# Kernel tuning notes

Measured on AMD Instinct MI355X. Metric: run time of the kernel, lower is better.

## Reference

```python
import jax, jax.numpy as jnp
import numpy as np

S = 2048  # expert group size
M = 768   # hidden size
H = 3072  # intermediate size
E = 16    # num experts


def top2_gating(gates):
    # gates: [G, S, E]
    G, S_, E_ = gates.shape
    C = 2 * S_ // E_
    mask_dtype = jnp.int32
    index_1 = jnp.argmax(gates, axis=-1)
    mask_1 = jax.nn.one_hot(index_1, E_, dtype=mask_dtype)
    gate_1 = jnp.einsum('GSE,GSE->GS', gates, mask_1)
    gates_without_top_1 = gates * (1 - mask_1)
    index_2 = jnp.argmax(gates_without_top_1, axis=-1)
    mask_2 = jax.nn.one_hot(index_2, E_, dtype=mask_dtype)
    gate_2 = jnp.einsum('GSE,GSE->GS', gates_without_top_1, mask_2)
    pos_1 = jnp.cumsum(mask_1, axis=-2) - mask_1
    mask_1 = mask_1 * (pos_1 < C)
    pos_1 = jnp.einsum('GSE,GSE->GS', pos_1, mask_1)
    mask_1_count = jnp.sum(mask_1, axis=-2)
    mask_1_flat = jnp.sum(mask_1, axis=-1)
    pos_2 = jnp.cumsum(mask_2, axis=-2) - mask_2 + jnp.expand_dims(mask_1_count, -2)
    mask_2 = mask_2 * (pos_2 < C)
    pos_2 = jnp.einsum('GSE,GSE->GS', pos_2, mask_2)
    mask_2_flat = jnp.sum(mask_2, axis=-1)
    gate_1 = gate_1 * mask_1_flat
    gate_2 = gate_2 * mask_2_flat
    denom = gate_1 + gate_2
    denom = jnp.where(denom > 0, denom, jnp.ones_like(denom))
    gate_1 = gate_1 / denom
    gate_2 = gate_2 / denom
    a = jnp.expand_dims(gate_1 * mask_1_flat, -1) * jax.nn.one_hot(index_1, E_, dtype=gates.dtype)
    b = jax.nn.one_hot(pos_1, C, dtype=gates.dtype)
    first = jnp.einsum('GSE,GSC->GSEC', a, b)
    a = jnp.expand_dims(gate_2 * mask_2_flat, -1) * jax.nn.one_hot(index_2, E_, dtype=gates.dtype)
    b = jax.nn.one_hot(pos_2, C, dtype=gates.dtype)
    second = jnp.einsum('GSE,GSC->GSEC', a, b)
    combined_tensor = first + second
    dispatch_tensor = combined_tensor.astype(jnp.bool_)
    return combined_tensor, dispatch_tensor


def setup_inputs() -> dict:
    key = jax.random.key(0)
    k1, k2, k3, k4 = jax.random.split(key, 4)
    inputs = jax.random.normal(k1, (4, 1024, M), dtype=jnp.float32)
    wg = jax.random.normal(k2, (M, E), dtype=jnp.float32) * (1.0 / np.sqrt(M))
    wi = jax.random.normal(k3, (E, M, H), dtype=jnp.float32) * (1.0 / np.sqrt(M))
    wo = jax.random.normal(k4, (E, H, M), dtype=jnp.float32) * (1.0 / np.sqrt(H))
    return {"inputs": inputs, "wg": wg, "wi": wi, "wo": wo}


def reference(inputs, wg, wi, wo):
    x = jnp.reshape(inputs, (-1, S, M))                      # [G, S, M]
    gates = jax.nn.softmax(jnp.einsum('GSM,ME->GSE', x, wg))
    combined_weights, dispatch_mask = top2_gating(gates)
    dispatched = jnp.einsum('GSEC,GSM->EGCM',
                            dispatch_mask.astype(x.dtype), x)
    h = jnp.einsum('EGCM,EMH->EGCH', dispatched, wi)
    h = jax.nn.relu(h)
    expert_out = jnp.einsum('EGCH,EHM->GECM', h, wo)
    out = jnp.einsum('GSEC,GECM->GSM', combined_weights, expert_out)
    return jnp.reshape(out, inputs.shape)
```

## Files before the change

kernel.cpp:

```cpp
#include <hip/hip_runtime.h>
#include <hip/hip_bf16.h>
#include <cstdint>
#include <cstddef>

#define S_TOK 2048
#define M_DIM 768
#define H_DIM 3072
#define E_NUM 16
#define CAP   256

using s16x8 = __attribute__((ext_vector_type(8))) short;
using f32x4 = __attribute__((ext_vector_type(4))) float;

__device__ __forceinline__ unsigned short f2bf(float f) {
    unsigned u = __float_as_uint(f);
    unsigned r = 0x7fffu + ((u >> 16) & 1u);
    return (unsigned short)((u + r) >> 16);
}

__device__ __forceinline__ void async16(const void* g, void* l) {
    __builtin_amdgcn_global_load_lds((const __attribute__((address_space(1))) void*)g,
                                     (__attribute__((address_space(3))) void*)l, 16, 0, 0);
}

__global__ void gating_kernel(const float* __restrict__ x, const float* __restrict__ wg,
                              int* __restrict__ e1o, int* __restrict__ e2o,
                              float* __restrict__ g1o, float* __restrict__ g2o, int ntok) {
    int gid  = blockIdx.x * blockDim.x + threadIdx.x;
    int tok  = gid >> 6;
    int lane = threadIdx.x & 63;
    if (tok >= ntok) return;
    const float* xr = x + (size_t)tok * M_DIM;
    float acc[E_NUM];
#pragma unroll
    for (int e = 0; e < E_NUM; ++e) acc[e] = 0.f;
    for (int m = lane; m < M_DIM; m += 64) {
        float xv = xr[m];
        const float* wr = wg + (size_t)m * E_NUM;
#pragma unroll
        for (int e = 0; e < E_NUM; ++e) acc[e] += xv * wr[e];
    }
#pragma unroll
    for (int off = 32; off >= 1; off >>= 1) {
#pragma unroll
        for (int e = 0; e < E_NUM; ++e) acc[e] += __shfl_xor(acc[e], off, 64);
    }
    if (lane == 0) {
        float mx = acc[0];
#pragma unroll
        for (int e = 1; e < E_NUM; ++e) mx = fmaxf(mx, acc[e]);
        float p[E_NUM]; float s = 0.f;
#pragma unroll
        for (int e = 0; e < E_NUM; ++e) { p[e] = expf(acc[e] - mx); s += p[e]; }
        float inv = 1.f / s;
        int b1 = 0; float v1 = -1.f;
#pragma unroll
        for (int e = 0; e < E_NUM; ++e) { if (p[e] > v1) { v1 = p[e]; b1 = e; } }
        int b2 = 0; float v2 = -1.f;
#pragma unroll
        for (int e = 0; e < E_NUM; ++e) { if (e != b1 && p[e] > v2) { v2 = p[e]; b2 = e; } }
        e1o[tok] = b1; e2o[tok] = b2;
        g1o[tok] = v1 * inv; g2o[tok] = v2 * inv;
    }
}

__global__ void assign_kernel(const int* __restrict__ e1a, const int* __restrict__ e2a,
                              const float* __restrict__ g1a, const float* __restrict__ g2a,
                              int* __restrict__ slot1, int* __restrict__ slot2,
                              float* __restrict__ w1, float* __restrict__ w2,
                              int* __restrict__ tfs, int G) {
    int g    = blockIdx.x;
    int tid  = threadIdx.x;
    int w    = tid >> 6;
    int lane = tid & 63;
    __shared__ int cnt1s[E_NUM];

    for (int i = tid; i < E_NUM * CAP; i += 1024) tfs[(size_t)g * E_NUM * CAP + i] = -1;
    __syncthreads();

    {
        int cnt = 0;
        for (int base = 0; base < S_TOK; base += 64) {
            int t = g * S_TOK + base + lane;
            bool pred = (e1a[t] == w);
            unsigned long long bal = __ballot(pred);
            int prefix = __popcll(bal & ((1ull << lane) - 1ull));
            if (pred) {
                int pos = cnt + prefix;
                if (pos < CAP) {
                    slot1[t] = w * CAP + pos;
                    tfs[((size_t)g * E_NUM + w) * CAP + pos] = base + lane;
                } else {
                    slot1[t] = -1;
                }
            }
            cnt += __popcll(bal);
        }
        if (lane == 0) cnt1s[w] = cnt < CAP ? cnt : CAP;
    }
    __syncthreads();
    {
        int cnt = cnt1s[w];
        for (int base = 0; base < S_TOK; base += 64) {
            int t = g * S_TOK + base + lane;
            bool pred = (e2a[t] == w);
            unsigned long long bal = __ballot(pred);
            int prefix = __popcll(bal & ((1ull << lane) - 1ull));
            if (pred) {
                int pos = cnt + prefix;
                if (pos < CAP) {
                    slot2[t] = w * CAP + pos;
                    tfs[((size_t)g * E_NUM + w) * CAP + pos] = base + lane;
                } else {
                    slot2[t] = -1;
                }
            }
            cnt += __popcll(bal);
        }
    }
    __syncthreads();
    for (int t = tid; t < S_TOK; t += 1024) {
        int gt = g * S_TOK + t;
        float a = slot1[gt] >= 0 ? g1a[gt] : 0.f;
        float b = slot2[gt] >= 0 ? g2a[gt] : 0.f;
        float denom = a + b;
        if (!(denom > 0.f)) denom = 1.f;
        w1[gt] = a / denom;
        w2[gt] = b / denom;
    }
}

__global__ void convert_x_kernel(const float* __restrict__ x, unsigned short* __restrict__ xb,
                                 int ntok) {
    int i4 = blockIdx.x * blockDim.x + threadIdx.x;
    size_t base = (size_t)i4 * 4;
    size_t n_real = (size_t)ntok * M_DIM;
    size_t n_tot  = (size_t)(ntok + 1) * M_DIM;
    if (base >= n_tot) return;
    ushort4 o;
    if (base < n_real) {
        float4 v = *(const float4*)&x[base];
        o.x = f2bf(v.x); o.y = f2bf(v.y); o.z = f2bf(v.z); o.w = f2bf(v.w);
    } else {
        o.x = o.y = o.z = o.w = 0;
    }
    *(ushort4*)&xb[base] = o;
}

__global__ __launch_bounds__(256) void transpose_conv_kernel(const float* __restrict__ src,
                                                             unsigned short* __restrict__ dst,
                                                             int R, int C) {
    __shared__ float T[64][65];
    int e  = blockIdx.z;
    int c0 = blockIdx.x * 64;
    int r0 = blockIdx.y * 64;
    int tid = threadIdx.x;
    int lx = tid & 63, ly = tid >> 6;
    const float* S = src + (size_t)e * R * C;
#pragma unroll
    for (int i = 0; i < 16; ++i) {
        int r = i * 4 + ly;
        T[r][lx] = S[(size_t)(r0 + r) * C + c0 + lx];
    }
    __syncthreads();
    unsigned short* D = dst + (size_t)e * C * R;
#pragma unroll
    for (int i = 0; i < 16; ++i) {
        int c = i * 4 + ly;
        D[(size_t)(c0 + c) * R + r0 + lx] = f2bf(T[lx][c]);
    }
}

template<int KLEN, bool GATHER>
__global__ __launch_bounds__(256) void mfma_gemm_kernel(
        const unsigned short* __restrict__ A,
        const unsigned short* __restrict__ B,
        const int* __restrict__ tfs,
        void* __restrict__ Out, int G, int N_total) {
    __shared__ unsigned short As[128 * 32];
    __shared__ unsigned short Bs[128 * 32];
    __shared__ int rowtok[128];

    int z  = blockIdx.z;
    int e  = z / G, g = z % G;
    int n0 = blockIdx.x * 128;
    int c0 = blockIdx.y * 128;
    int tid = threadIdx.x;

    if (GATHER) {
        if (tid < 128) rowtok[tid] = tfs[((size_t)g * E_NUM + e) * CAP + c0 + tid];
        __syncthreads();
    }

    int r4 = tid >> 2, l4 = tid & 3;
    const unsigned short *apt0, *apt1;
    if (GATHER) {
        int t0 = rowtok[r4], t1 = rowtok[64 + r4];
        size_t row0 = (t0 < 0) ? (size_t)(G * S_TOK) : (size_t)(g * S_TOK + t0);
        size_t row1 = (t1 < 0) ? (size_t)(G * S_TOK) : (size_t)(g * S_TOK + t1);
        apt0 = A + row0 * KLEN + l4 * 8;
        apt1 = A + row1 * KLEN + l4 * 8;
    } else {
        apt0 = A + ((size_t)z * CAP + c0 + r4) * KLEN + l4 * 8;
        apt1 = apt0 + (size_t)64 * KLEN;
    }
    const unsigned short* Bexp = B + (size_t)e * N_total * KLEN;
    const unsigned short* bpt0 = Bexp + ((size_t)n0 + r4) * KLEN + l4 * 8;
    const unsigned short* bpt1 = bpt0 + (size_t)64 * KLEN;

    int wv = tid >> 6;
    unsigned short* as0 = &As[(wv * 16) * 32];
    unsigned short* as1 = &As[(64 + wv * 16) * 32];
    unsigned short* bs0 = &Bs[(wv * 16) * 32];
    unsigned short* bs1 = &Bs[(64 + wv * 16) * 32];

    int lane = tid & 63;
    int r = lane & 15, q = lane >> 4;
    int wm = wv & 1, wn = wv >> 1;

    f32x4 acc[4][4];
#pragma unroll
    for (int i = 0; i < 4; ++i)
#pragma unroll
        for (int j = 0; j < 4; ++j) acc[i][j] = (f32x4)(0.f);

    for (int k0 = 0; k0 < KLEN; k0 += 32) {
        async16(apt0, as0);
        async16(apt1, as1);
        async16(bpt0, bs0);
        async16(bpt1, bs1);
        apt0 += 32; apt1 += 32; bpt0 += 32; bpt1 += 32;
        __syncthreads();
        s16x8 af[4], bfr[4];
#pragma unroll
        for (int i = 0; i < 4; ++i)
            af[i] = *(const s16x8*)&As[(wm * 64 + i * 16 + r) * 32 + q * 8];
#pragma unroll
        for (int j = 0; j < 4; ++j)
            bfr[j] = *(const s16x8*)&Bs[(wn * 64 + j * 16 + r) * 32 + q * 8];
#pragma unroll
        for (int i = 0; i < 4; ++i)
#pragma unroll
            for (int j = 0; j < 4; ++j)
                acc[i][j] = __builtin_amdgcn_mfma_f32_16x16x32_bf16(af[i], bfr[j], acc[i][j], 0, 0, 0);
        __syncthreads();
    }

    if (GATHER) {
        unsigned short* H = (unsigned short*)Out;
#pragma unroll
        for (int i = 0; i < 4; ++i) {
#pragma unroll
            for (int v = 0; v < 4; ++v) {
                int m_loc = wm * 64 + i * 16 + q * 4 + v;
                unsigned short* row = H + ((size_t)z * CAP + c0 + m_loc) * N_total + n0;
#pragma unroll
                for (int j = 0; j < 4; ++j) {
                    int n_loc = wn * 64 + j * 16 + r;
                    row[n_loc] = f2bf(fmaxf(acc[i][j][v], 0.f));
                }
            }
        }
    } else {
        float* O = (float*)Out;
#pragma unroll
        for (int i = 0; i < 4; ++i) {
#pragma unroll
            for (int v = 0; v < 4; ++v) {
                int m_loc = wm * 64 + i * 16 + q * 4 + v;
                float* row = O + (((size_t)g * E_NUM + e) * CAP + c0 + m_loc) * N_total + n0;
#pragma unroll
                for (int j = 0; j < 4; ++j) {
                    int n_loc = wn * 64 + j * 16 + r;
                    row[n_loc] = acc[i][j][v];
                }
            }
        }
    }
}

__global__ void combine_kernel(const float* __restrict__ eo,
                               const int* __restrict__ slot1, const int* __restrict__ slot2,
                               const float* __restrict__ w1, const float* __restrict__ w2,
                               float* __restrict__ out, int G) {
    int t = blockIdx.x;
    int g = t / S_TOK;
    int tid = threadIdx.x;
    int s1 = slot1[t], s2 = slot2[t];
    float a = w1[t], b = w2[t];
    const float* base_g = eo + (size_t)g * E_NUM * CAP * M_DIM;
    const float* p1 = base_g + (size_t)(s1 < 0 ? 0 : s1) * M_DIM;
    const float* p2 = base_g + (size_t)(s2 < 0 ? 0 : s2) * M_DIM;
    for (int m = tid; m < M_DIM; m += 256) {
        float v = 0.f;
        if (s1 >= 0) v += a * p1[m];
        if (s2 >= 0) v += b * p2[m];
        out[(size_t)t * M_DIM + m] = v;
    }
}

extern "C" void kernel_launch(void* const* d_in, const int* in_sizes, int n_in,
                              void* d_out, int out_size, void* d_ws, size_t ws_size,
                              hipStream_t stream) {
    const float* x  = (const float*)d_in[0];
    const float* wg = (const float*)d_in[1];
    const float* wi = (const float*)d_in[2];
    const float* wo = (const float*)d_in[3];
    float* out = (float*)d_out;

    int ntok = in_sizes[0] / M_DIM;
    int G = ntok / S_TOK;

    char* wsp = (char*)d_ws;
    auto carve = [&](size_t bytes) {
        void* p = (void*)wsp;
        wsp += (bytes + 255) & ~(size_t)255;
        return p;
    };
    int*   e1    = (int*)carve((size_t)ntok * 4);
    int*   e2    = (int*)carve((size_t)ntok * 4);
    float* g1    = (float*)carve((size_t)ntok * 4);
    float* g2    = (float*)carve((size_t)ntok * 4);
    int*   slot1 = (int*)carve((size_t)ntok * 4);
    int*   slot2 = (int*)carve((size_t)ntok * 4);
    float* w1    = (float*)carve((size_t)ntok * 4);
    float* w2    = (float*)carve((size_t)ntok * 4);
    int*   tfs   = (int*)carve((size_t)G * E_NUM * CAP * 4);
    unsigned short* xb  = (unsigned short*)carve((size_t)(ntok + 1) * M_DIM * 2);
    unsigned short* wiT = (unsigned short*)carve((size_t)E_NUM * H_DIM * M_DIM * 2);
    unsigned short* woT = (unsigned short*)carve((size_t)E_NUM * M_DIM * H_DIM * 2);
    unsigned short* h   = (unsigned short*)carve((size_t)E_NUM * G * CAP * H_DIM * 2);
    float* eo = (float*)carve((size_t)G * E_NUM * CAP * M_DIM * 4);

    gating_kernel<<<(ntok * 64 + 255) / 256, 256, 0, stream>>>(x, wg, e1, e2, g1, g2, ntok);
    assign_kernel<<<G, 1024, 0, stream>>>(e1, e2, g1, g2, slot1, slot2, w1, w2, tfs, G);

    int nx4 = ((ntok + 1) * M_DIM) / 4;
    convert_x_kernel<<<(nx4 + 255) / 256, 256, 0, stream>>>(x, xb, ntok);
    transpose_conv_kernel<<<dim3(H_DIM / 64, M_DIM / 64, E_NUM), 256, 0, stream>>>(wi, wiT, M_DIM, H_DIM);
    transpose_conv_kernel<<<dim3(M_DIM / 64, H_DIM / 64, E_NUM), 256, 0, stream>>>(wo, woT, H_DIM, M_DIM);

    mfma_gemm_kernel<M_DIM, true><<<dim3(H_DIM / 128, CAP / 128, E_NUM * G), 256, 0, stream>>>(
        xb, wiT, tfs, h, G, H_DIM);
    mfma_gemm_kernel<H_DIM, false><<<dim3(M_DIM / 128, CAP / 128, E_NUM * G), 256, 0, stream>>>(
        h, woT, tfs, eo, G, M_DIM);

    combine_kernel<<<ntok, 256, 0, stream>>>(eo, slot1, slot2, w1, w2, out, G);
}
```

Measured before the change: 552.4 us.

## Fuse combine into second GEMM via atomics, split-K, fuse x conversion into gating

The second expert GEMM now splits K in two and atomically accumulates gate-weighted results directly into the output, removing the expert-output buffer and the combine kernel. A small zero kernel clears the output first. The bf16 conversion of x is folded into the gating kernel, and the first GEMM uses 256-row tiles with 512 threads to reuse weight tiles across capacity rows. This trades a buffer round trip and a few launches for float atomics, which are nondeterministic in summation order, and it hardcodes two groups in the grid indexing.

```diff
diff --git a/kernel.cpp b/kernel.cpp
--- a/kernel.cpp
+++ b/kernel.cpp
@@ -25,17 +25,24 @@
 
 __global__ void gating_kernel(const float* __restrict__ x, const float* __restrict__ wg,
                               int* __restrict__ e1o, int* __restrict__ e2o,
-                              float* __restrict__ g1o, float* __restrict__ g2o, int ntok) {
+                              float* __restrict__ g1o, float* __restrict__ g2o,
+                              unsigned short* __restrict__ xb, int ntok) {
+    if (blockIdx.x == 0) {
+        for (int m = threadIdx.x; m < M_DIM; m += blockDim.x)
+            xb[(size_t)ntok * M_DIM + m] = 0;
+    }
     int gid  = blockIdx.x * blockDim.x + threadIdx.x;
     int tok  = gid >> 6;
     int lane = threadIdx.x & 63;
     if (tok >= ntok) return;
     const float* xr = x + (size_t)tok * M_DIM;
+    unsigned short* xbr = xb + (size_t)tok * M_DIM;
     float acc[E_NUM];
 #pragma unroll
     for (int e = 0; e < E_NUM; ++e) acc[e] = 0.f;
     for (int m = lane; m < M_DIM; m += 64) {
         float xv = xr[m];
+        xbr[m] = f2bf(xv);
         const float* wr = wg + (size_t)m * E_NUM;
 #pragma unroll
         for (int e = 0; e < E_NUM; ++e) acc[e] += xv * wr[e];
@@ -67,7 +74,7 @@
 __global__ void assign_kernel(const int* __restrict__ e1a, const int* __restrict__ e2a,
                               const float* __restrict__ g1a, const float* __restrict__ g2a,
                               int* __restrict__ slot1, int* __restrict__ slot2,
-                              float* __restrict__ w1, float* __restrict__ w2,
+                              float* __restrict__ wslot,
                               int* __restrict__ tfs, int G) {
     int g    = blockIdx.x;
     int tid  = threadIdx.x;
@@ -79,10 +86,15 @@
     __syncthreads();
 
     {
+        int vals[S_TOK / 64];
+#pragma unroll
+        for (int it = 0; it < S_TOK / 64; ++it) vals[it] = e1a[g * S_TOK + it * 64 + lane];
         int cnt = 0;
-        for (int base = 0; base < S_TOK; base += 64) {
+#pragma unroll
+        for (int it = 0; it < S_TOK / 64; ++it) {
+            int base = it * 64;
             int t = g * S_TOK + base + lane;
-            bool pred = (e1a[t] == w);
+            bool pred = (vals[it] == w);
             unsigned long long bal = __ballot(pred);
             int prefix = __popcll(bal & ((1ull << lane) - 1ull));
             if (pred) {
@@ -100,10 +112,15 @@
     }
     __syncthreads();
     {
+        int vals[S_TOK / 64];
+#pragma unroll
+        for (int it = 0; it < S_TOK / 64; ++it) vals[it] = e2a[g * S_TOK + it * 64 + lane];
         int cnt = cnt1s[w];
-        for (int base = 0; base < S_TOK; base += 64) {
+#pragma unroll
+        for (int it = 0; it < S_TOK / 64; ++it) {
+            int base = it * 64;
             int t = g * S_TOK + base + lane;
-            bool pred = (e2a[t] == w);
+            bool pred = (vals[it] == w);
             unsigned long long bal = __ballot(pred);
             int prefix = __popcll(bal & ((1ull << lane) - 1ull));
             if (pred) {
@@ -121,30 +138,14 @@
     __syncthreads();
     for (int t = tid; t < S_TOK; t += 1024) {
         int gt = g * S_TOK + t;
-        float a = slot1[gt] >= 0 ? g1a[gt] : 0.f;
-        float b = slot2[gt] >= 0 ? g2a[gt] : 0.f;
+        int s1 = slot1[gt], s2 = slot2[gt];
+        float a = s1 >= 0 ? g1a[gt] : 0.f;
+        float b = s2 >= 0 ? g2a[gt] : 0.f;
         float denom = a + b;
         if (!(denom > 0.f)) denom = 1.f;
-        w1[gt] = a / denom;
-        w2[gt] = b / denom;
-    }
-}
-
-__global__ void convert_x_kernel(const float* __restrict__ x, unsigned short* __restrict__ xb,
-                                 int ntok) {
-    int i4 = blockIdx.x * blockDim.x + threadIdx.x;
-    size_t base = (size_t)i4 * 4;
-    size_t n_real = (size_t)ntok * M_DIM;
-    size_t n_tot  = (size_t)(ntok + 1) * M_DIM;
-    if (base >= n_tot) return;
-    ushort4 o;
-    if (base < n_real) {
-        float4 v = *(const float4*)&x[base];
-        o.x = f2bf(v.x); o.y = f2bf(v.y); o.z = f2bf(v.z); o.w = f2bf(v.w);
-    } else {
-        o.x = o.y = o.z = o.w = 0;
-    }
-    *(ushort4*)&xb[base] = o;
+        if (s1 >= 0) wslot[(size_t)g * E_NUM * CAP + s1] = a / denom;
+        if (s2 >= 0) wslot[(size_t)g * E_NUM * CAP + s2] = b / denom;
+    }
 }
 
 __global__ __launch_bounds__(256) void transpose_conv_kernel(const float* __restrict__ src,
@@ -171,42 +172,120 @@
     }
 }
 
-template<int KLEN, bool GATHER>
-__global__ __launch_bounds__(256) void mfma_gemm_kernel(
+__global__ __launch_bounds__(512) void gemm1_kernel(
         const unsigned short* __restrict__ A,
         const unsigned short* __restrict__ B,
         const int* __restrict__ tfs,
-        void* __restrict__ Out, int G, int N_total) {
+        unsigned short* __restrict__ Hout, int G) {
+    __shared__ unsigned short As[256 * 32];
+    __shared__ unsigned short Bs[128 * 32];
+    __shared__ int rowtok[256];
+
+    int e  = blockIdx.z;
+    int n0 = (blockIdx.x >> 1) * 128;
+    int g  = blockIdx.x & 1;
+    int z  = e * G + g;
+    int tid = threadIdx.x;
+
+    if (tid < 256) rowtok[tid] = tfs[((size_t)g * E_NUM + e) * CAP + tid];
+    __syncthreads();
+
+    int r4 = tid >> 2, l4 = tid & 3;
+    int t0 = rowtok[r4], t1 = rowtok[128 + r4];
+    size_t row0 = (t0 < 0) ? (size_t)(G * S_TOK) : (size_t)(g * S_TOK + t0);
+    size_t row1 = (t1 < 0) ? (size_t)(G * S_TOK) : (size_t)(g * S_TOK + t1);
+    const unsigned short* apt0 = A + row0 * M_DIM + l4 * 8;
+    const unsigned short* apt1 = A + row1 * M_DIM + l4 * 8;
+    const unsigned short* bpt  = B + (size_t)e * H_DIM * M_DIM + ((size_t)n0 + r4) * M_DIM + l4 * 8;
+
+    int wv = tid >> 6;
+    unsigned short* as0 = &As[(wv * 16) * 32];
+    unsigned short* as1 = &As[(128 + wv * 16) * 32];
+    unsigned short* bs  = &Bs[(wv * 16) * 32];
+
+    int lane = tid & 63;
+    int r = lane & 15, q = lane >> 4;
+    int wm = wv & 3, wn = wv >> 2;
+
+    f32x4 acc[4][4];
+#pragma unroll
+    for (int i = 0; i < 4; ++i)
+#pragma unroll
+        for (int j = 0; j < 4; ++j) acc[i][j] = (f32x4)(0.f);
+
+    for (int k0 = 0; k0 < M_DIM; k0 += 32) {
+        async16(apt0, as0);
+        async16(apt1, as1);
+        async16(bpt, bs);
+        apt0 += 32; apt1 += 32; bpt += 32;
+        __syncthreads();
+        s16x8 af[4], bfr[4];
+#pragma unroll
+        for (int i = 0; i < 4; ++i)
+            af[i] = *(const s16x8*)&As[(wm * 64 + i * 16 + r) * 32 + q * 8];
+#pragma unroll
+        for (int j = 0; j < 4; ++j)
+            bfr[j] = *(const s16x8*)&Bs[(wn * 64 + j * 16 + r) * 32 + q * 8];
+#pragma unroll
+        for (int i = 0; i < 4; ++i)
+#pragma unroll
+            for (int j = 0; j < 4; ++j)
+                acc[i][j] = __builtin_amdgcn_mfma_f32_16x16x32_bf16(af[i], bfr[j], acc[i][j], 0, 0, 0);
+        __syncthreads();
+    }
+
+#pragma unroll
+    for (int i = 0; i < 4; ++i) {
+#pragma unroll
+        for (int v = 0; v < 4; ++v) {
+            int m_loc = wm * 64 + i * 16 + q * 4 + v;
+            unsigned short* row = Hout + ((size_t)z * CAP + m_loc) * H_DIM + n0;
+#pragma unroll
+            for (int j = 0; j < 4; ++j) {
+                int n_loc = wn * 64 + j * 16 + r;
+                row[n_loc] = f2bf(fmaxf(acc[i][j][v], 0.f));
+            }
+        }
+    }
+}
+
+__global__ void zero_kernel(float4* __restrict__ p, int n4) {
+    int i = blockIdx.x * blockDim.x + threadIdx.x;
+    if (i < n4) p[i] = make_float4(0.f, 0.f, 0.f, 0.f);
+}
+
+__global__ __launch_bounds__(256) void gemm2_kernel(
+        const unsigned short* __restrict__ A,
+        const unsigned short* __restrict__ B,
+        const int* __restrict__ tfs,
+        const float* __restrict__ wslot,
+        float* __restrict__ out, int G) {
     __shared__ unsigned short As[128 * 32];
     __shared__ unsigned short Bs[128 * 32];
-    __shared__ int rowtok[128];
-
-    int z  = blockIdx.z;
-    int e  = z / G, g = z % G;
+    __shared__ int   rowtok[128];
+    __shared__ float rowwt[128];
+
+    int e  = blockIdx.z & 15;
+    int kc = blockIdx.z >> 4;
     int n0 = blockIdx.x * 128;
-    int c0 = blockIdx.y * 128;
+    int c0 = (blockIdx.y >> 1) * 128;
+    int g  = blockIdx.y & 1;
+    int z  = e * G + g;
     int tid = threadIdx.x;
 
-    if (GATHER) {
-        if (tid < 128) rowtok[tid] = tfs[((size_t)g * E_NUM + e) * CAP + c0 + tid];
-        __syncthreads();
-    }
-
+    if (tid < 128) {
+        size_t sidx = ((size_t)g * E_NUM + e) * CAP + c0 + tid;
+        rowtok[tid] = tfs[sidx];
+        rowwt[tid]  = wslot[sidx];
+    }
+
+    const int KC = H_DIM / 2;
+    int kb = kc * KC;
     int r4 = tid >> 2, l4 = tid & 3;
-    const unsigned short *apt0, *apt1;
-    if (GATHER) {
-        int t0 = rowtok[r4], t1 = rowtok[64 + r4];
-        size_t row0 = (t0 < 0) ? (size_t)(G * S_TOK) : (size_t)(g * S_TOK + t0);
-        size_t row1 = (t1 < 0) ? (size_t)(G * S_TOK) : (size_t)(g * S_TOK + t1);
-        apt0 = A + row0 * KLEN + l4 * 8;
-        apt1 = A + row1 * KLEN + l4 * 8;
-    } else {
-        apt0 = A + ((size_t)z * CAP + c0 + r4) * KLEN + l4 * 8;
-        apt1 = apt0 + (size_t)64 * KLEN;
-    }
-    const unsigned short* Bexp = B + (size_t)e * N_total * KLEN;
-    const unsigned short* bpt0 = Bexp + ((size_t)n0 + r4) * KLEN + l4 * 8;
-    const unsigned short* bpt1 = bpt0 + (size_t)64 * KLEN;
+    const unsigned short* apt0 = A + ((size_t)z * CAP + c0 + r4) * H_DIM + kb + l4 * 8;
+    const unsigned short* apt1 = apt0 + (size_t)64 * H_DIM;
+    const unsigned short* bpt0 = B + (size_t)e * M_DIM * H_DIM + ((size_t)n0 + r4) * H_DIM + kb + l4 * 8;
+    const unsigned short* bpt1 = bpt0 + (size_t)64 * H_DIM;
 
     int wv = tid >> 6;
     unsigned short* as0 = &As[(wv * 16) * 32];
@@ -224,7 +303,7 @@
 #pragma unroll
         for (int j = 0; j < 4; ++j) acc[i][j] = (f32x4)(0.f);
 
-    for (int k0 = 0; k0 < KLEN; k0 += 32) {
+    for (int k0 = 0; k0 < KC; k0 += 32) {
         async16(apt0, as0);
         async16(apt1, as1);
         async16(bpt0, bs0);
@@ -246,56 +325,21 @@
         __syncthreads();
     }
 
-    if (GATHER) {
-        unsigned short* H = (unsigned short*)Out;
-#pragma unroll
-        for (int i = 0; i < 4; ++i) {
-#pragma unroll
-            for (int v = 0; v < 4; ++v) {
-                int m_loc = wm * 64 + i * 16 + q * 4 + v;
-                unsigned short* row = H + ((size_t)z * CAP + c0 + m_loc) * N_total + n0;
-#pragma unroll
-                for (int j = 0; j < 4; ++j) {
-                    int n_loc = wn * 64 + j * 16 + r;
-                    row[n_loc] = f2bf(fmaxf(acc[i][j][v], 0.f));
-                }
+#pragma unroll
+    for (int i = 0; i < 4; ++i) {
+#pragma unroll
+        for (int v = 0; v < 4; ++v) {
+            int m_loc = wm * 64 + i * 16 + q * 4 + v;
+            int tok = rowtok[m_loc];
+            if (tok < 0) continue;
+            float w = rowwt[m_loc];
+            float* orow = out + ((size_t)(g * S_TOK + tok)) * M_DIM + n0;
+#pragma unroll
+            for (int j = 0; j < 4; ++j) {
+                int n_loc = wn * 64 + j * 16 + r;
+                atomicAdd(&orow[n_loc], w * acc[i][j][v]);
             }
         }
-    } else {
-        float* O = (float*)Out;
-#pragma unroll
-        for (int i = 0; i < 4; ++i) {
-#pragma unroll
-            for (int v = 0; v < 4; ++v) {
-                int m_loc = wm * 64 + i * 16 + q * 4 + v;
-                float* row = O + (((size_t)g * E_NUM + e) * CAP + c0 + m_loc) * N_total + n0;
-#pragma unroll
-                for (int j = 0; j < 4; ++j) {
-                    int n_loc = wn * 64 + j * 16 + r;
-                    row[n_loc] = acc[i][j][v];
-                }
-            }
-        }
-    }
-}
-
-__global__ void combine_kernel(const float* __restrict__ eo,
-                               const int* __restrict__ slot1, const int* __restrict__ slot2,
-                               const float* __restrict__ w1, const float* __restrict__ w2,
-                               float* __restrict__ out, int G) {
-    int t = blockIdx.x;
-    int g = t / S_TOK;
-    int tid = threadIdx.x;
-    int s1 = slot1[t], s2 = slot2[t];
-    float a = w1[t], b = w2[t];
-    const float* base_g = eo + (size_t)g * E_NUM * CAP * M_DIM;
-    const float* p1 = base_g + (size_t)(s1 < 0 ? 0 : s1) * M_DIM;
-    const float* p2 = base_g + (size_t)(s2 < 0 ? 0 : s2) * M_DIM;
-    for (int m = tid; m < M_DIM; m += 256) {
-        float v = 0.f;
-        if (s1 >= 0) v += a * p1[m];
-        if (s2 >= 0) v += b * p2[m];
-        out[(size_t)t * M_DIM + m] = v;
     }
 }
 
@@ -323,27 +367,23 @@
     float* g2    = (float*)carve((size_t)ntok * 4);
     int*   slot1 = (int*)carve((size_t)ntok * 4);
     int*   slot2 = (int*)carve((size_t)ntok * 4);
-    float* w1    = (float*)carve((size_t)ntok * 4);
-    float* w2    = (float*)carve((size_t)ntok * 4);
+    float* wslot = (float*)carve((size_t)G * E_NUM * CAP * 4);
     int*   tfs   = (int*)carve((size_t)G * E_NUM * CAP * 4);
     unsigned short* xb  = (unsigned short*)carve((size_t)(ntok + 1) * M_DIM * 2);
     unsigned short* wiT = (unsigned short*)carve((size_t)E_NUM * H_DIM * M_DIM * 2);
     unsigned short* woT = (unsigned short*)carve((size_t)E_NUM * M_DIM * H_DIM * 2);
     unsigned short* h   = (unsigned short*)carve((size_t)E_NUM * G * CAP * H_DIM * 2);
-    float* eo = (float*)carve((size_t)G * E_NUM * CAP * M_DIM * 4);
-
-    gating_kernel<<<(ntok * 64 + 255) / 256, 256, 0, stream>>>(x, wg, e1, e2, g1, g2, ntok);
-    assign_kernel<<<G, 1024, 0, stream>>>(e1, e2, g1, g2, slot1, slot2, w1, w2, tfs, G);
-
-    int nx4 = ((ntok + 1) * M_DIM) / 4;
-    convert_x_kernel<<<(nx4 + 255) / 256, 256, 0, stream>>>(x, xb, ntok);
+
+    gating_kernel<<<(ntok * 64 + 255) / 256, 256, 0, stream>>>(x, wg, e1, e2, g1, g2, xb, ntok);
+    assign_kernel<<<G, 1024, 0, stream>>>(e1, e2, g1, g2, slot1, slot2, wslot, tfs, G);
+
     transpose_conv_kernel<<<dim3(H_DIM / 64, M_DIM / 64, E_NUM), 256, 0, stream>>>(wi, wiT, M_DIM, H_DIM);
     transpose_conv_kernel<<<dim3(M_DIM / 64, H_DIM / 64, E_NUM), 256, 0, stream>>>(wo, woT, H_DIM, M_DIM);
 
-    mfma_gemm_kernel<M_DIM, true><<<dim3(H_DIM / 128, CAP / 128, E_NUM * G), 256, 0, stream>>>(
-        xb, wiT, tfs, h, G, H_DIM);
-    mfma_gemm_kernel<H_DIM, false><<<dim3(M_DIM / 128, CAP / 128, E_NUM * G), 256, 0, stream>>>(
-        h, woT, tfs, eo, G, M_DIM);
-
-    combine_kernel<<<ntok, 256, 0, stream>>>(eo, slot1, slot2, w1, w2, out, G);
-}
+    gemm1_kernel<<<dim3((H_DIM / 128) * 2, 1, E_NUM), 512, 0, stream>>>(xb, wiT, tfs, h, G);
+
+    int n4 = ntok * M_DIM / 4;
+    zero_kernel<<<(n4 + 255) / 256, 256, 0, stream>>>((float4*)out, n4);
+
+    gemm2_kernel<<<dim3(M_DIM / 128, 2 * 2, 2 * E_NUM), 256, 0, stream>>>(h, woT, tfs, wslot, out, G);
+}
```

After: 567.8 us. 1.03x slower.
